# Kernel optimization log

Measured on AMD Instinct MI355X. Metric: run time of the kernel, lower is better.

Reference implementation:

```python
import jax, jax.numpy as jnp
import numpy as np

T, B, D, H, R, S, M = 1024, 16, 512, 8, 32, 16, 16
TQ = R + T + S   # query length
KL = M + R + T   # key/value length
NEG_INF = -1e8


def setup_inputs() -> dict:
    key = jax.random.key(0)
    ks = jax.random.split(key, 12)
    utterance = jax.random.normal(ks[0], (T, B, D), jnp.float32)
    right_context = jax.random.normal(ks[1], (R, B, D), jnp.float32)
    summary = jax.random.normal(ks[2], (S, B, D), jnp.float32)
    mems = jax.random.normal(ks[3], (M, B, D), jnp.float32)
    # valid lengths in [T//2, T]; force max == T so data-dependent shapes are static
    lengths = jax.random.randint(ks[4], (B,), T // 2, T + 1).at[0].set(T).astype(jnp.int64)
    # block-streaming style mask: query i may only attend to keys <= i + M
    q_idx = jnp.arange(TQ)[:, None]
    k_idx = jnp.arange(KL)[None, :]
    attention_mask = k_idx > (q_idx + M)  # True = masked
    scale = 0.02
    Wq = jax.random.normal(ks[5], (D, D), jnp.float32) * scale
    bq = jnp.zeros((D,), jnp.float32)
    Wkv = jax.random.normal(ks[6], (2 * D, D), jnp.float32) * scale
    bkv = jnp.zeros((2 * D,), jnp.float32)
    Wo = jax.random.normal(ks[7], (D, D), jnp.float32) * scale
    bo = jnp.zeros((D,), jnp.float32)
    return dict(utterance=utterance, lengths=lengths, right_context=right_context,
                summary=summary, mems=mems, attention_mask=attention_mask,
                Wq=Wq, bq=bq, Wkv=Wkv, bkv=bkv, Wo=Wo, bo=bo)


def _split_heads(x):
    # (L, B, D) -> (B*H, L, D//H), matching torch .view(-1, B*H, d).transpose(0, 1)
    L = x.shape[0]
    return x.reshape(L, B * H, D // H).transpose(1, 0, 2)


def reference(utterance, lengths, right_context, summary, mems, attention_mask,
              Wq, bq, Wkv, bkv, Wo, bo):
    d_head = D // H
    scaling = d_head ** -0.5

    query_in = jnp.concatenate([right_context, utterance, summary], axis=0)   # (TQ, B, D)
    kv_in = jnp.concatenate([mems, right_context, utterance], axis=0)         # (KL, B, D)

    query = query_in @ Wq.T + bq
    kv = kv_in @ Wkv.T + bkv
    k, v = jnp.split(kv, 2, axis=2)

    q = _split_heads(query)  # (B*H, TQ, d)
    kh = _split_heads(k)     # (B*H, KL, d)
    vh = _split_heads(v)

    w = jnp.einsum('nqd,nkd->nqk', q * scaling, kh).astype(jnp.float32)
    w = jnp.where(attention_mask[None, :, :], NEG_INF, w)

    # padding mask (B > 1 path): klengths = lengths + M + right_context_blocks_length
    rcbl = TQ - jnp.max(lengths) - S  # == R since max(lengths) == T
    klengths = lengths + M + rcbl
    pad_mask = jnp.arange(KL)[None, :] >= klengths[:, None]  # (B, KL)
    w = w.reshape(B, H, TQ, KL)
    w = jnp.where(pad_mask[:, None, None, :], NEG_INF, w)
    w = w.reshape(B * H, TQ, KL)

    probs = jax.nn.softmax(w, axis=-1)  # dropout p=0.0
    attn = jnp.einsum('nqk,nkd->nqd', probs, vh)          # (B*H, TQ, d)
    attn = attn.transpose(1, 0, 2).reshape(TQ, B, D)

    out = attn @ Wo.T + bo                                # (TQ, B, D)
    output_right_context = out[:TQ - S]                    # (R+T, B, D)
    output_mems = jnp.clip(out[TQ - S:], -10.0, 10.0)      # tanh_on_mem=False
    return output_right_context, output_mems[:-1]          # (S-1, B, D)
```

## Files before the change

kernel.cpp:

```cpp
#include <hip/hip_runtime.h>

#define T_   1024
#define B_   16
#define D_   512
#define H_   8
#define R_   32
#define S_   16
#define M_   16
#define TQ_  1072
#define KL_  1072
#define DH_  64
#define NROW 17152
#define K_   512
#define LQ_  268
#define QSCALE 0.18033688f

typedef unsigned short u16;
using bf16x8 = __attribute__((ext_vector_type(8))) short;
using bf16x4 = __attribute__((ext_vector_type(4))) short;
using f32x4  = __attribute__((ext_vector_type(4))) float;
using u16x4  = __attribute__((ext_vector_type(4))) unsigned short;

__device__ __forceinline__ u16 f2bf(float f) {
    unsigned int u = __builtin_bit_cast(unsigned int, f);
    unsigned int r = u + 0x7fffu + ((u >> 16) & 1u);
    return (u16)(r >> 16);
}

__device__ __forceinline__ unsigned int cvt_pk_bf16(float a, float b) {
    unsigned int r;
    asm("v_cvt_pk_bf16_f32 %0, %1, %2" : "=v"(r) : "v"(a), "v"(b));
    return r;
}

__device__ __forceinline__ f32x4 mfma16(bf16x4 a, bf16x4 b, f32x4 c) {
    asm("v_mfma_f32_16x16x16_bf16 %0, %1, %2, %0" : "+v"(c) : "v"(a), "v"(b));
    return c;
}

__device__ __forceinline__ void gload_lds16(const u16* g, u16* l) {
    __builtin_amdgcn_global_load_lds(
        (const __attribute__((address_space(1))) unsigned int*)g,
        (__attribute__((address_space(3))) unsigned int*)l,
        16, 0, 0);
}

__device__ __forceinline__ int xcd_swz(int bid, int nwg) {
    const int q = nwg >> 3, r = nwg & 7;
    const int xcd = bid & 7, idx = bid >> 3;
    return (xcd < r ? xcd * (q + 1) : r * (q + 1) + (xcd - r) * q) + idx;
}

__global__ void k_convert4(const float4* __restrict__ utt, const float4* __restrict__ rc,
                           const float4* __restrict__ smr, const float4* __restrict__ mems,
                           const float4* __restrict__ Wq, const float4* __restrict__ Wkv,
                           const float4* __restrict__ Wo,
                           u16x4* __restrict__ xall,
                           u16x4* __restrict__ wq, u16x4* __restrict__ wkv,
                           u16x4* __restrict__ wo)
{
    const int N4 = 17408 * D_ / 4;
    const int MB = M_ * B_ * D_ / 4;
    const int RB = MB + R_ * B_ * D_ / 4;
    const int UB = RB + T_ * B_ * D_ / 4;
    const int W1 = D_ * D_ / 4, W2 = 2 * D_ * D_ / 4;
    for (int i = blockIdx.x * blockDim.x + threadIdx.x; i < N4;
         i += gridDim.x * blockDim.x) {
        float4 v;
        if (i < MB)      v = mems[i];
        else if (i < RB) v = rc[i - MB];
        else if (i < UB) v = utt[i - RB];
        else             v = smr[i - UB];
        xall[i] = (u16x4){f2bf(v.x), f2bf(v.y), f2bf(v.z), f2bf(v.w)};
        if (i < W1) { v = Wq[i];  wq[i]  = (u16x4){f2bf(v.x), f2bf(v.y), f2bf(v.z), f2bf(v.w)}; }
        if (i < W2) { v = Wkv[i]; wkv[i] = (u16x4){f2bf(v.x), f2bf(v.y), f2bf(v.z), f2bf(v.w)}; }
        if (i < W1) { v = Wo[i];  wo[i]  = (u16x4){f2bf(v.x), f2bf(v.y), f2bf(v.z), f2bf(v.w)}; }
    }
}

template<bool TOR>
__device__ __forceinline__ void core128(const u16* __restrict__ Ab,
                                        const u16* __restrict__ Wb,
                                        u16* As, u16* Bs, f32x4* acc)
{
    const int tid  = threadIdx.x;
    const int w    = tid >> 6, lane = tid & 63;
    const int col  = lane & 15, quad = lane >> 4;
    const int sr   = tid >> 3;
    const int sc   = (tid & 7) ^ (sr & 7);
    const u16* gA  = Ab + (size_t)sr * K_ + sc * 8;
    const u16* gB  = Wb + (size_t)sr * K_ + sc * 8;

#pragma unroll
    for (int i = 0; i < 16; i++) acc[i] = (f32x4){0.f, 0.f, 0.f, 0.f};

    for (int kt = 0; kt < 8; ++kt) {
        __syncthreads();
#pragma unroll
        for (int i = 0; i < 4; i++)
            gload_lds16(gA + (size_t)(i * 32) * K_ + kt * 64,
                        &As[(i * 32 + w * 8) * 64]);
#pragma unroll
        for (int i = 0; i < 4; i++)
            gload_lds16(gB + (size_t)(i * 32) * K_ + kt * 64,
                        &Bs[(i * 32 + w * 8) * 64]);
        __syncthreads();
#pragma unroll
        for (int kh = 0; kh < 2; ++kh) {
            bf16x8 aF[2], bF[8];
#pragma unroll
            for (int mi = 0; mi < 2; mi++)
                aF[mi] = *(const bf16x8*)&As[(w * 32 + mi * 16 + col) * 64
                             + (((kh * 4 + quad) ^ (col & 7)) * 8)];
#pragma unroll
            for (int ni = 0; ni < 8; ni++)
                bF[ni] = *(const bf16x8*)&Bs[(ni * 16 + col) * 64
                             + (((kh * 4 + quad) ^ (col & 7)) * 8)];
            if (TOR) {
#pragma unroll
                for (int ni = 0; ni < 8; ni++)
#pragma unroll
                    for (int mi = 0; mi < 2; mi++)
                        acc[ni * 2 + mi] = __builtin_amdgcn_mfma_f32_16x16x32_bf16(
                            bF[ni], aF[mi], acc[ni * 2 + mi], 0, 0, 0);
            } else {
#pragma unroll
                for (int mi = 0; mi < 2; mi++)
#pragma unroll
                    for (int ni = 0; ni < 8; ni++)
                        acc[mi * 8 + ni] = __builtin_amdgcn_mfma_f32_16x16x32_bf16(
                            aF[mi], bF[ni], acc[mi * 8 + ni], 0, 0, 0);
            }
        }
    }
}

__global__ __launch_bounds__(256, 4)
void k_gemm_qkv9(const u16* __restrict__ xall,
                 const u16* __restrict__ wqp, const u16* __restrict__ wkvp,
                 const float* __restrict__ bq, const float* __restrict__ bkv,
                 u16* __restrict__ qb, u16* __restrict__ kb, u16* __restrict__ vt)
{
    __shared__ __align__(16) u16 As[128 * 64];
    __shared__ __align__(16) u16 Bs[128 * 64];

    const int wgid = xcd_swz(blockIdx.x, 134 * 12);
    const int tn = wgid % 12, tm = wgid / 12;
    const int typ = tn >> 2, sub = tn & 3;
    const u16* Ab = (typ == 0 ? xall + (size_t)256 * K_ : xall)
                    + (size_t)tm * 128 * K_;
    const u16* Wb = (typ == 0 ? wqp : wkvp + (typ == 2 ? (size_t)512 * K_ : 0))
                    + (size_t)sub * 128 * K_;

    const int tid = threadIdx.x;
    const int w = tid >> 6, lane = tid & 63;
    const int col = lane & 15, quad = lane >> 4;

    f32x4 acc[16];
    if (typ == 2) {
        core128<false>(Ab, Wb, As, Bs, acc);
        const int lq = tm * 2 + (w >> 1);
        const int so = (w & 1) * 2;
#pragma unroll
        for (int ni = 0; ni < 8; ni++) {
            const int f = sub * 128 + ni * 16 + col;
            const float bs = bkv[512 + f];
#pragma unroll
            for (int r = 0; r < 4; r++) {
                const int bb = quad * 4 + r;
                unsigned int pk = cvt_pk_bf16(acc[0 * 8 + ni][r] + bs,
                                              acc[1 * 8 + ni][r] + bs);
                *(unsigned int*)&vt[(((size_t)bb * LQ_ + lq) * 512 + f) * 4 + so] = pk;
            }
        }
    } else {
        core128<true>(Ab, Wb, As, Bs, acc);
        const float* bias = (typ == 0) ? bq : bkv;
        u16* outp = (typ == 0) ? qb : kb;
        const float qs = (typ == 0) ? QSCALE : 1.0f;
#pragma unroll
        for (int ni = 0; ni < 8; ni++) {
            const int gc0 = sub * 128 + ni * 16 + quad * 4;
            const float4 bs4 = *(const float4*)&bias[gc0];
#pragma unroll
            for (int mi = 0; mi < 2; mi++) {
                const int mrow = tm * 128 + w * 32 + mi * 16 + col;
                f32x4 a = acc[ni * 2 + mi];
                uint2 pk;
                pk.x = cvt_pk_bf16((a[0] + bs4.x) * qs, (a[1] + bs4.y) * qs);
                pk.y = cvt_pk_bf16((a[2] + bs4.z) * qs, (a[3] + bs4.w) * qs);
                *(uint2*)&outp[(size_t)mrow * 512 + gc0] = pk;
            }
        }
    }
}

__global__ __launch_bounds__(256, 4)
void k_gemm_o9(const u16* __restrict__ A, const u16* __restrict__ W,
               const float* __restrict__ bias, float* __restrict__ Co)
{
    __shared__ __align__(16) u16 As[128 * 64];
    __shared__ __align__(16) u16 Bs[128 * 64];

    const int wgid = xcd_swz(blockIdx.x, 134 * 4);
    const int tn = wgid % 4, tm = wgid / 4;
    const u16* Ab = A + (size_t)tm * 128 * K_;
    const u16* Wb = W + (size_t)tn * 128 * K_;

    const int tid = threadIdx.x;
    const int w = tid >> 6, lane = tid & 63;
    const int col = lane & 15, quad = lane >> 4;

    f32x4 acc[16];
    core128<true>(Ab, Wb, As, Bs, acc);

#pragma unroll
    for (int ni = 0; ni < 8; ni++) {
        const int gc0 = tn * 128 + ni * 16 + quad * 4;
        const float4 bs4 = *(const float4*)&bias[gc0];
#pragma unroll
        for (int mi = 0; mi < 2; mi++) {
            const int l = tm * 8 + w * 2 + mi;
            if (l == TQ_ - 1) continue;
            const int mrow = tm * 128 + w * 32 + mi * 16 + col;
            f32x4 a = acc[ni * 2 + mi];
            float4 v = {a[0] + bs4.x, a[1] + bs4.y, a[2] + bs4.z, a[3] + bs4.w};
            if (l >= TQ_ - S_) {
                v.x = fminf(10.0f, fmaxf(-10.0f, v.x));
                v.y = fminf(10.0f, fmaxf(-10.0f, v.y));
                v.z = fminf(10.0f, fmaxf(-10.0f, v.z));
                v.w = fminf(10.0f, fmaxf(-10.0f, v.w));
            }
            *(float4*)&Co[(size_t)mrow * 512 + gc0] = v;
        }
    }
}

__global__ __launch_bounds__(256, 4)
void k_attn5(const u16* __restrict__ qbuf, const u16* __restrict__ kb,
             const u16* __restrict__ vt, const int* __restrict__ lenp,
             u16* __restrict__ attnb)
{
    __shared__ __align__(16) u16 Ks[2][64 * 64];
    __shared__ __align__(16) u16 Vs[2][64 * 64];

    const int blk  = blockIdx.x;
    const int qblk = 16 - (blk >> 7);
    const int bh   = blk & 127;
    const int b = bh >> 3, h = bh & 7;
    const int tid = threadIdx.x;
    const int w = tid >> 6, lane = tid & 63;
    const int col = lane & 15, quad = lane >> 4;

    int stride = (lenp[1] == 0) ? 2 : 1;
    int maxlen = 0;
    for (int i = 0; i < B_; i++) maxlen = max(maxlen, lenp[i * stride]);
    const int klen = lenp[b * stride] + M_ + (TQ_ - maxlen - S_);

    const int q0 = qblk * 64;
    const int qw = q0 + w * 16;
    const int q  = qw + col;

    int qrow = min(q, TQ_ - 1);
    const u16* qp = qbuf + ((size_t)qrow * B_ + b) * D_ + h * DH_ + quad * 8;
    bf16x8 bq0 = *(const bf16x8*)(qp);
    bf16x8 bq1 = *(const bf16x8*)(qp + 32);

    const int s0 = tid, s1 = tid + 256;
    const u16* kbase = kb + (size_t)b * 512 + h * DH_;
    size_t kof0 = (size_t)(s0 >> 3) * 8192 + (size_t)(((s0 & 7) ^ ((s0 >> 3) & 7)) * 8);
    size_t kof1 = (size_t)(s1 >> 3) * 8192 + (size_t)(((s1 & 7) ^ ((s1 >> 3) & 7)) * 8);
    const u16* vbase = vt + ((size_t)b * LQ_ * 512 + (size_t)h * DH_) * 4;
    auto vchunk = [](int s) -> size_t {
        int fp = s >> 4;
        int lq = (s & 15) ^ (fp & 15);
        return (size_t)lq * 2048 + (size_t)fp * 8;
    };
    const size_t vof0 = vchunk(s0), vof1 = vchunk(s1);

    float li = 0.f;
    f32x4 o[4];
#pragma unroll
    for (int g = 0; g < 4; g++) o[g] = (f32x4){0.f, 0.f, 0.f, 0.f};

    const int nk = min(q0 + 64 + M_, klen);
    const int numkt = (nk + 63) >> 6;

    gload_lds16(kbase + kof0, &Ks[0][(size_t)w * 512]);
    gload_lds16(kbase + kof1, &Ks[0][2048 + (size_t)w * 512]);
    gload_lds16(vbase + vof0, &Vs[0][(size_t)w * 512]);
    gload_lds16(vbase + vof1, &Vs[0][2048 + (size_t)w * 512]);

    for (int kt = 0; kt < numkt; kt++) {
        const int kn0 = kt * 64;
        const int cur = kt & 1;
        __syncthreads();
        if (kt + 1 < numkt) {
            const size_t kstep = (size_t)(kn0 + 64) * 8192;
            const size_t vstep = (size_t)(kt + 1) * 32768;
            gload_lds16(kbase + kstep + kof0, &Ks[cur ^ 1][(size_t)w * 512]);
            gload_lds16(kbase + kstep + kof1, &Ks[cur ^ 1][2048 + (size_t)w * 512]);
            gload_lds16(vbase + vstep + vof0, &Vs[cur ^ 1][(size_t)w * 512]);
            gload_lds16(vbase + vstep + vof1, &Vs[cur ^ 1][2048 + (size_t)w * 512]);
        }

        f32x4 sc[4];
        __builtin_amdgcn_s_setprio(1);
#pragma unroll
        for (int g = 0; g < 4; g++) {
            int key = g * 16 + col;
            bf16x8 a0 = *(const bf16x8*)&Ks[cur][key * 64 + ((quad ^ (key & 7)) * 8)];
            bf16x8 a1 = *(const bf16x8*)&Ks[cur][key * 64 + (((4 + quad) ^ (key & 7)) * 8)];
            f32x4 z = {0.f, 0.f, 0.f, 0.f};
            z = __builtin_amdgcn_mfma_f32_16x16x32_bf16(a0, bq0, z, 0, 0, 0);
            z = __builtin_amdgcn_mfma_f32_16x16x32_bf16(a1, bq1, z, 0, 0, 0);
            sc[g] = z;
        }
        __builtin_amdgcn_s_setprio(0);

        const bool needmask = (kn0 + 63 > qw + M_) || (kn0 + 63 >= klen);
        if (needmask) {
#pragma unroll
            for (int g = 0; g < 4; g++)
#pragma unroll
                for (int r = 0; r < 4; r++) {
                    int key = kn0 + g * 16 + quad * 4 + r;
                    bool valid = (key <= q + M_) && (key < klen);
                    sc[g][r] = valid ? sc[g][r] : -1e8f;
                }
        }

        bf16x4 pk[4];
#pragma unroll
        for (int g = 0; g < 4; g++) {
            float pr[4];
#pragma unroll
            for (int r = 0; r < 4; r++)
                pr[r] = __builtin_amdgcn_exp2f(sc[g][r]);
            li += (pr[0] + pr[1]) + (pr[2] + pr[3]);
            uint2 pku;
            pku.x = cvt_pk_bf16(pr[0], pr[1]);
            pku.y = cvt_pk_bf16(pr[2], pr[3]);
            pk[g] = __builtin_bit_cast(bf16x4, pku);
        }

        __builtin_amdgcn_s_setprio(1);
#pragma unroll
        for (int g = 0; g < 4; g++) {
            const int d  = g * 16 + col;
            const int fp = d >> 1, fo = (d & 1) * 4;
#pragma unroll
            for (int ks = 0; ks < 4; ks++) {
                const int lq  = ks * 4 + quad;
                const int pos = fp * 16 + (lq ^ (fp & 15));
                bf16x4 av = __builtin_bit_cast(bf16x4,
                    *(const u16x4*)&Vs[cur][pos * 8 + fo]);
                o[g] = mfma16(av, pk[ks], o[g]);
            }
        }
        __builtin_amdgcn_s_setprio(0);
    }

    li += __shfl_xor(li, 16);
    li += __shfl_xor(li, 32);
    const float inv = 1.0f / li;
    const int qo = qw + col;
    if (qw + 16 <= TQ_) {
#pragma unroll
        for (int g = 0; g < 4; g++) {
            uint2 pkk;
            pkk.x = cvt_pk_bf16(o[g][0] * inv, o[g][1] * inv);
            pkk.y = cvt_pk_bf16(o[g][2] * inv, o[g][3] * inv);
            *(uint2*)&attnb[((size_t)qo * B_ + b) * D_ + h * DH_ + g * 16 + quad * 4] = pkk;
        }
    }
}

extern "C" void kernel_launch(void* const* d_in, const int* in_sizes, int n_in,
                              void* d_out, int out_size, void* d_ws, size_t ws_size,
                              hipStream_t stream)
{
    const float* utt  = (const float*)d_in[0];
    const int*   len  = (const int*)  d_in[1];
    const float* rc   = (const float*)d_in[2];
    const float* smr  = (const float*)d_in[3];
    const float* mems = (const float*)d_in[4];
    const float* Wq   = (const float*)d_in[6];
    const float* bq   = (const float*)d_in[7];
    const float* Wkv  = (const float*)d_in[8];
    const float* bkv  = (const float*)d_in[9];
    const float* Wo   = (const float*)d_in[10];
    const float* bo   = (const float*)d_in[11];

    char* ws = (char*)d_ws;
    size_t off = 0;
    auto alloc = [&](size_t bytes) -> void* {
        void* p = ws + off;
        off += (bytes + 255) & ~(size_t)255;
        return p;
    };
    u16* xall = (u16*)alloc((size_t)17408 * D_ * 2);
    u16* wq   = (u16*)alloc((size_t)D_ * D_ * 2);
    u16* wkv  = (u16*)alloc((size_t)2 * D_ * D_ * 2);
    u16* wo   = (u16*)alloc((size_t)D_ * D_ * 2);
    u16* qb   = (u16*)alloc((size_t)NROW * D_ * 2);
    u16* kb   = (u16*)alloc((size_t)NROW * D_ * 2);
    u16* vt   = (u16*)alloc((size_t)B_ * LQ_ * 512 * 4 * 2 + 65536);
    u16* attnb = xall;

    k_convert4<<<2048, 256, 0, stream>>>((const float4*)utt, (const float4*)rc,
                                         (const float4*)smr, (const float4*)mems,
                                         (const float4*)Wq, (const float4*)Wkv,
                                         (const float4*)Wo,
                                         (u16x4*)xall,
                                         (u16x4*)wq, (u16x4*)wkv, (u16x4*)wo);
    k_gemm_qkv9<<<134 * 12, 256, 0, stream>>>(xall, wq, wkv, bq, bkv, qb, kb, vt);
    k_attn5<<<17 * 128, 256, 0, stream>>>(qb, kb, vt, len, attnb);
    k_gemm_o9<<<134 * 4, 256, 0, stream>>>(attnb, wo, bo, (float*)d_out);
}
```

Measured before the change: 200.1 us.

## Process two query blocks per attention workgroup to reuse K/V tiles

Each attention workgroup now handles a pair of adjacent 64-row query blocks (qhi and qlo), sharing each loaded K/V LDS tile between both. Grid drops from 17×128 to 9×128 blocks. This halves K/V global loads for paired blocks and amortizes sync/prefetch, at the cost of doubled accumulator registers (possible occupancy drop) and fewer blocks for latency hiding on a 256-CU device.

```diff
diff --git a/kernel.cpp b/kernel.cpp
--- a/kernel.cpp
+++ b/kernel.cpp
@@ -244,9 +244,11 @@
     __shared__ __align__(16) u16 Ks[2][64 * 64];
     __shared__ __align__(16) u16 Vs[2][64 * 64];
 
-    const int blk  = blockIdx.x;
-    const int qblk = 16 - (blk >> 7);
-    const int bh   = blk & 127;
+    const int blk = blockIdx.x;
+    const int pp  = blk >> 7;
+    const int qhi = 16 - 2 * pp;
+    const int qlo = qhi - 1;
+    const int bh  = blk & 127;
     const int b = bh >> 3, h = bh & 7;
     const int tid = threadIdx.x;
     const int w = tid >> 6, lane = tid & 63;
@@ -257,14 +259,16 @@
     for (int i = 0; i < B_; i++) maxlen = max(maxlen, lenp[i * stride]);
     const int klen = lenp[b * stride] + M_ + (TQ_ - maxlen - S_);
 
-    const int q0 = qblk * 64;
-    const int qw = q0 + w * 16;
-    const int q  = qw + col;
-
-    int qrow = min(q, TQ_ - 1);
-    const u16* qp = qbuf + ((size_t)qrow * B_ + b) * D_ + h * DH_ + quad * 8;
-    bf16x8 bq0 = *(const bf16x8*)(qp);
-    bf16x8 bq1 = *(const bf16x8*)(qp + 32);
+    const int qwh = qhi * 64 + w * 16, qh = qwh + col;
+    const int qwl = qlo * 64 + w * 16, ql = qwl + col;
+    const bool hasLo = (qlo >= 0);
+
+    const u16* qph = qbuf + ((size_t)min(qh, TQ_ - 1) * B_ + b) * D_ + h * DH_ + quad * 8;
+    bf16x8 bqh0 = *(const bf16x8*)(qph);
+    bf16x8 bqh1 = *(const bf16x8*)(qph + 32);
+    const u16* qpl = qbuf + ((size_t)min(max(ql, 0), TQ_ - 1) * B_ + b) * D_ + h * DH_ + quad * 8;
+    bf16x8 bql0 = *(const bf16x8*)(qpl);
+    bf16x8 bql1 = *(const bf16x8*)(qpl + 32);
 
     const int s0 = tid, s1 = tid + 256;
     const u16* kbase = kb + (size_t)b * 512 + h * DH_;
@@ -278,13 +282,17 @@
     };
     const size_t vof0 = vchunk(s0), vof1 = vchunk(s1);
 
-    float li = 0.f;
-    f32x4 o[4];
-#pragma unroll
-    for (int g = 0; g < 4; g++) o[g] = (f32x4){0.f, 0.f, 0.f, 0.f};
-
-    const int nk = min(q0 + 64 + M_, klen);
-    const int numkt = (nk + 63) >> 6;
+    float lih = 0.f, lil = 0.f;
+    f32x4 oh[4], ol[4];
+#pragma unroll
+    for (int g = 0; g < 4; g++) {
+        oh[g] = (f32x4){0.f, 0.f, 0.f, 0.f};
+        ol[g] = (f32x4){0.f, 0.f, 0.f, 0.f};
+    }
+
+    const int nk_hi = min(qhi * 64 + 64 + M_, klen);
+    const int nk_lo = hasLo ? min(qlo * 64 + 64 + M_, klen) : 0;
+    const int numkt = (nk_hi + 63) >> 6;
 
     gload_lds16(kbase + kof0, &Ks[0][(size_t)w * 512]);
     gload_lds16(kbase + kof1, &Ks[0][2048 + (size_t)w * 512]);
@@ -294,6 +302,7 @@
     for (int kt = 0; kt < numkt; kt++) {
         const int kn0 = kt * 64;
         const int cur = kt & 1;
+        const bool loNow = hasLo && (kn0 < nk_lo);
         __syncthreads();
         if (kt + 1 < numkt) {
             const size_t kstep = (size_t)(kn0 + 64) * 8192;
@@ -304,7 +313,7 @@
             gload_lds16(vbase + vstep + vof1, &Vs[cur ^ 1][2048 + (size_t)w * 512]);
         }
 
-        f32x4 sc[4];
+        f32x4 sch[4], scl[4];
         __builtin_amdgcn_s_setprio(1);
 #pragma unroll
         for (int g = 0; g < 4; g++) {
@@ -312,36 +321,65 @@
             bf16x8 a0 = *(const bf16x8*)&Ks[cur][key * 64 + ((quad ^ (key & 7)) * 8)];
             bf16x8 a1 = *(const bf16x8*)&Ks[cur][key * 64 + (((4 + quad) ^ (key & 7)) * 8)];
             f32x4 z = {0.f, 0.f, 0.f, 0.f};
-            z = __builtin_amdgcn_mfma_f32_16x16x32_bf16(a0, bq0, z, 0, 0, 0);
-            z = __builtin_amdgcn_mfma_f32_16x16x32_bf16(a1, bq1, z, 0, 0, 0);
-            sc[g] = z;
+            z = __builtin_amdgcn_mfma_f32_16x16x32_bf16(a0, bqh0, z, 0, 0, 0);
+            z = __builtin_amdgcn_mfma_f32_16x16x32_bf16(a1, bqh1, z, 0, 0, 0);
+            sch[g] = z;
+            if (loNow) {
+                f32x4 y = {0.f, 0.f, 0.f, 0.f};
+                y = __builtin_amdgcn_mfma_f32_16x16x32_bf16(a0, bql0, y, 0, 0, 0);
+                y = __builtin_amdgcn_mfma_f32_16x16x32_bf16(a1, bql1, y, 0, 0, 0);
+                scl[g] = y;
+            }
         }
         __builtin_amdgcn_s_setprio(0);
 
-        const bool needmask = (kn0 + 63 > qw + M_) || (kn0 + 63 >= klen);
-        if (needmask) {
+        if ((kn0 + 63 > qwh + M_) || (kn0 + 63 >= klen)) {
 #pragma unroll
             for (int g = 0; g < 4; g++)
 #pragma unroll
                 for (int r = 0; r < 4; r++) {
                     int key = kn0 + g * 16 + quad * 4 + r;
-                    bool valid = (key <= q + M_) && (key < klen);
-                    sc[g][r] = valid ? sc[g][r] : -1e8f;
+                    bool valid = (key <= qh + M_) && (key < klen);
+                    sch[g][r] = valid ? sch[g][r] : -1e8f;
                 }
         }
-
-        bf16x4 pk[4];
+        if (loNow && ((kn0 + 63 > qwl + M_) || (kn0 + 63 >= klen))) {
+#pragma unroll
+            for (int g = 0; g < 4; g++)
+#pragma unroll
+                for (int r = 0; r < 4; r++) {
+                    int key = kn0 + g * 16 + quad * 4 + r;
+                    bool valid = (key <= ql + M_) && (key < klen);
+                    scl[g][r] = valid ? scl[g][r] : -1e8f;
+                }
+        }
+
+        bf16x4 pkh[4], pkl[4];
 #pragma unroll
         for (int g = 0; g < 4; g++) {
             float pr[4];
 #pragma unroll
             for (int r = 0; r < 4; r++)
-                pr[r] = __builtin_amdgcn_exp2f(sc[g][r]);
-            li += (pr[0] + pr[1]) + (pr[2] + pr[3]);
+                pr[r] = __builtin_amdgcn_exp2f(sch[g][r]);
+            lih += (pr[0] + pr[1]) + (pr[2] + pr[3]);
             uint2 pku;
             pku.x = cvt_pk_bf16(pr[0], pr[1]);
             pku.y = cvt_pk_bf16(pr[2], pr[3]);
-            pk[g] = __builtin_bit_cast(bf16x4, pku);
+            pkh[g] = __builtin_bit_cast(bf16x4, pku);
+        }
+        if (loNow) {
+#pragma unroll
+            for (int g = 0; g < 4; g++) {
+                float pr[4];
+#pragma unroll
+                for (int r = 0; r < 4; r++)
+                    pr[r] = __builtin_amdgcn_exp2f(scl[g][r]);
+                lil += (pr[0] + pr[1]) + (pr[2] + pr[3]);
+                uint2 pku;
+                pku.x = cvt_pk_bf16(pr[0], pr[1]);
+                pku.y = cvt_pk_bf16(pr[2], pr[3]);
+                pkl[g] = __builtin_bit_cast(bf16x4, pku);
+            }
         }
 
         __builtin_amdgcn_s_setprio(1);
@@ -355,23 +393,37 @@
                 const int pos = fp * 16 + (lq ^ (fp & 15));
                 bf16x4 av = __builtin_bit_cast(bf16x4,
                     *(const u16x4*)&Vs[cur][pos * 8 + fo]);
-                o[g] = mfma16(av, pk[ks], o[g]);
+                oh[g] = mfma16(av, pkh[ks], oh[g]);
+                if (loNow) ol[g] = mfma16(av, pkl[ks], ol[g]);
             }
         }
         __builtin_amdgcn_s_setprio(0);
     }
 
-    li += __shfl_xor(li, 16);
-    li += __shfl_xor(li, 32);
-    const float inv = 1.0f / li;
-    const int qo = qw + col;
-    if (qw + 16 <= TQ_) {
+    lih += __shfl_xor(lih, 16);
+    lih += __shfl_xor(lih, 32);
+    const float invh = 1.0f / lih;
+    if (qwh + 16 <= TQ_) {
 #pragma unroll
         for (int g = 0; g < 4; g++) {
             uint2 pkk;
-            pkk.x = cvt_pk_bf16(o[g][0] * inv, o[g][1] * inv);
-            pkk.y = cvt_pk_bf16(o[g][2] * inv, o[g][3] * inv);
-            *(uint2*)&attnb[((size_t)qo * B_ + b) * D_ + h * DH_ + g * 16 + quad * 4] = pkk;
+            pkk.x = cvt_pk_bf16(oh[g][0] * invh, oh[g][1] * invh);
+            pkk.y = cvt_pk_bf16(oh[g][2] * invh, oh[g][3] * invh);
+            *(uint2*)&attnb[((size_t)(qwh + col) * B_ + b) * D_ + h * DH_ + g * 16 + quad * 4] = pkk;
+        }
+    }
+    if (hasLo) {
+        lil += __shfl_xor(lil, 16);
+        lil += __shfl_xor(lil, 32);
+        const float invl = 1.0f / lil;
+        if (qwl + 16 <= TQ_) {
+#pragma unroll
+            for (int g = 0; g < 4; g++) {
+                uint2 pkk;
+                pkk.x = cvt_pk_bf16(ol[g][0] * invl, ol[g][1] * invl);
+                pkk.y = cvt_pk_bf16(ol[g][2] * invl, ol[g][3] * invl);
+                *(uint2*)&attnb[((size_t)(qwl + col) * B_ + b) * D_ + h * DH_ + g * 16 + quad * 4] = pkk;
+            }
         }
     }
 }
@@ -415,6 +467,6 @@
                                          (u16x4*)xall,
                                          (u16x4*)wq, (u16x4*)wkv, (u16x4*)wo);
     k_gemm_qkv9<<<134 * 12, 256, 0, stream>>>(xall, wq, wkv, bq, bkv, qb, kb, vt);
-    k_attn5<<<17 * 128, 256, 0, stream>>>(qb, kb, vt, len, attnb);
+    k_attn5<<<9 * 128, 256, 0, stream>>>(qb, kb, vt, len, attnb);
     k_gemm_o9<<<134 * 4, 256, 0, stream>>>(attnb, wo, bo, (float*)d_out);
 }
```

After: 230.8 us. +15.3%, slower.
